# Kernel optimization log

Hardware: AMD Instinct MI355X
Metric: run time of the kernel (lower is better)

Reference implementation:

```python
import jax, jax.numpy as jnp
import numpy as np
from jax import lax

D_CONV = 4


def setup_inputs() -> dict:
    key = jax.random.key(0)
    ks = jax.random.split(key, 8)
    b, L, d_model = 2, 1024, 1024
    d_inner, d_state = 2048, 16
    s = 0.02  # weight scale
    return {
        "x": jax.random.normal(ks[0], (b, L, d_model), jnp.float32),
        "in_w": jax.random.normal(ks[1], (2 * d_inner, d_model), jnp.float32) * s,
        "in_b": jnp.zeros((2 * d_inner,), jnp.float32),
        "conv_w": jax.random.normal(ks[2], (d_inner, 1, D_CONV), jnp.float32) * s,
        "conv_b": jnp.zeros((d_inner,), jnp.float32),
        "xproj_w": jax.random.normal(ks[3], (2 * d_state + 1, d_inner), jnp.float32) * s,
        "dt_w": jax.random.normal(ks[4], (d_inner, 1), jnp.float32) * s,
        "dt_b": jnp.zeros((d_inner,), jnp.float32),
        "A_log": jax.random.normal(ks[5], (d_inner, d_state), jnp.float32),
        "D": jnp.ones((d_inner,), jnp.float32),
        "out_w": jax.random.normal(ks[6], (d_model, d_inner), jnp.float32) * s,
    }


def reference(x, in_w, in_b, conv_w, conv_b, xproj_w, dt_w, dt_b, A_log, D, out_w):
    b, L, _ = x.shape
    d_inner = conv_w.shape[0]
    d_state = A_log.shape[1]

    xz = x @ in_w.T + in_b                       # (b, L, 2*d_inner)
    xh, z = jnp.split(xz, 2, axis=-1)            # each (b, L, d_inner)

    # depthwise causal conv1d (torch pads d_conv-1 both sides then slices [:L])
    xc = jnp.transpose(xh, (0, 2, 1))            # (b, d_inner, L)
    xc = lax.conv_general_dilated(
        xc, conv_w, window_strides=(1,), padding=[(D_CONV - 1, 0)],
        feature_group_count=d_inner, dimension_numbers=("NCH", "OIH", "NCH"))
    xc = xc + conv_b[None, :, None]
    xh = jnp.transpose(xc, (0, 2, 1))            # (b, L, d_inner)

    xh = xh * jax.nn.silu(z)

    proj = xh @ xproj_w.T                        # (b, L, 2*d_state+1)
    dlt = proj[..., :1]                          # (b, L, 1)
    B = proj[..., 1:1 + d_state]                 # (b, L, d_state)
    C = proj[..., 1 + d_state:]                  # (b, L, d_state)

    # dt_proj: (b,L,1) -> (b,L,d_inner); source applies softplus then exp
    delta = jnp.exp(jax.nn.softplus(dlt @ dt_w.T + dt_b))  # (b, L, d_inner)

    A = -jnp.exp(A_log)                          # (d_inner, d_state)

    def step(h, inp):
        xt, dt, Bt, Ct = inp                     # (b,i), (b,i), (b,s), (b,s)
        A_bar = jnp.exp(A[None] * dt[..., None])          # (b, i, s)
        B_bar = dt[..., None] * Bt[:, None, :]            # (b, i, s)
        h = A_bar * h + B_bar * xt[..., None]             # (b, i, s)
        yt = jnp.einsum("bis,bs->bi", h, Ct)              # (b, i)
        return h, yt

    h0 = jnp.zeros((b, d_inner, d_state), x.dtype)
    xs = (jnp.moveaxis(xh, 1, 0), jnp.moveaxis(delta, 1, 0),
          jnp.moveaxis(B, 1, 0), jnp.moveaxis(C, 1, 0))
    _, ys = lax.scan(step, h0, xs)               # (L, b, d_inner)
    y = jnp.moveaxis(ys, 0, 1) + D * xh          # (b, L, d_inner)

    return y @ out_w.T                           # (b, L, d_model)
```

## Files before the change

kernel.cpp:

```cpp
#include <hip/hip_runtime.h>
#include <hip/hip_bf16.h>

#define NTOK   2048
#define DMODEL 1024
#define DINNER 2048
#define DSTATE 16
#define SEQLEN 1024
#define NPROJ  33
#define NPAD   48
#define KSPLIT 16
#define CCH    64
#define CT     16

typedef __attribute__((ext_vector_type(8))) short bf16x8;
typedef __attribute__((ext_vector_type(4))) float f32x4;
typedef __attribute__((ext_vector_type(8))) unsigned short us8;

__device__ __forceinline__ unsigned short f2bf(float f) {
  unsigned u = __float_as_uint(f);
  return (unsigned short)((u + 0x7FFFu + ((u >> 16) & 1u)) >> 16);
}

__device__ __forceinline__ void gload_lds16(const void* g, void* l) {
  __builtin_amdgcn_global_load_lds(
      (const __attribute__((address_space(1))) unsigned int*)g,
      (__attribute__((address_space(3))) unsigned int*)l, 16, 0, 0);
}

#define CAST_N0 (NTOK * DMODEL)
#define CAST_N1 (CAST_N0 + 2 * DINNER * DMODEL)
#define CAST_N2 (CAST_N1 + DMODEL * DINNER)
#define CAST_N3 (CAST_N2 + NPAD * DINNER)
__global__ __launch_bounds__(256) void cast4_bf16_kernel(
    const float* __restrict__ s0, const float* __restrict__ s1,
    const float* __restrict__ s2, const float* __restrict__ s3,
    unsigned short* __restrict__ dst) {
  const int idx = (blockIdx.x * 256 + threadIdx.x) * 8;
  const float* src;
  int off;
  if (idx < CAST_N0) { src = s0; off = idx; }
  else if (idx < CAST_N1) { src = s1; off = idx - CAST_N0; }
  else if (idx < CAST_N2) { src = s2; off = idx - CAST_N1; }
  else {
    off = idx - CAST_N2;
    if (off >= NPROJ * DINNER) {
      us8 z = {0, 0, 0, 0, 0, 0, 0, 0};
      *(us8*)(dst + idx) = z;
      return;
    }
    src = s3;
  }
  const float4 a = *(const float4*)(src + off);
  const float4 b = *(const float4*)(src + off + 4);
  us8 o;
  o[0] = f2bf(a.x); o[1] = f2bf(a.y); o[2] = f2bf(a.z); o[3] = f2bf(a.w);
  o[4] = f2bf(b.x); o[5] = f2bf(b.y); o[6] = f2bf(b.z); o[7] = f2bf(b.w);
  *(us8*)(dst + idx) = o;
}

template <int BN>
__global__ __launch_bounds__(256) void gemm_bt_mfma(
    const unsigned short* __restrict__ A, const unsigned short* __restrict__ B,
    const float* __restrict__ bias, float* __restrict__ C, int M, int K) {
  constexpr int TN = BN / 32;
  __shared__ unsigned short As[2][128 * 32];
  __shared__ unsigned short Bs[2][BN * 32];

  const int tid = threadIdx.x;
  const int wid = tid >> 6;
  const int lane = tid & 63;
  const int n0 = blockIdx.x * 128;
  const int m0 = blockIdx.y * BN;

  const int wave_m = wid & 1;
  const int wave_n = wid >> 1;
  const int lm = lane & 15;
  const int lq = lane >> 4;

  f32x4 acc[4][TN] = {};

  for (int k0 = 0; k0 < K; k0 += 64) {
    __syncthreads();
#pragma unroll
    for (int h = 0; h < 2; ++h) {
      const int kh = k0 + h * 32;
#pragma unroll
      for (int j = 0; j < 2; ++j) {
        const int cb = j * 256 + wid * 64;
        const int c = cb + lane;
        gload_lds16(A + (size_t)(n0 + (c >> 2)) * K + kh + (c & 3) * 8,
                    &As[h][cb * 8]);
      }
#pragma unroll
      for (int j = 0; j < BN / 64; ++j) {
        const int cb = j * 256 + wid * 64;
        const int c = cb + lane;
        gload_lds16(B + (size_t)(m0 + (c >> 2)) * K + kh + (c & 3) * 8,
                    &Bs[h][cb * 8]);
      }
    }
    __syncthreads();

#pragma unroll
    for (int h = 0; h < 2; ++h) {
      bf16x8 af[4], bfr[TN];
#pragma unroll
      for (int tm = 0; tm < 4; ++tm)
        af[tm] = *(const bf16x8*)
            &As[h][(wave_m * 64 + tm * 16 + lm) * 32 + lq * 8];
#pragma unroll
      for (int tn = 0; tn < TN; ++tn)
        bfr[tn] = *(const bf16x8*)
            &Bs[h][(wave_n * (BN / 2) + tn * 16 + lm) * 32 + lq * 8];
#pragma unroll
      for (int tm = 0; tm < 4; ++tm)
#pragma unroll
        for (int tn = 0; tn < TN; ++tn)
          acc[tm][tn] = __builtin_amdgcn_mfma_f32_16x16x32_bf16(
              af[tm], bfr[tn], acc[tm][tn], 0, 0, 0);
    }
  }

#pragma unroll
  for (int tm = 0; tm < 4; ++tm) {
    const int row = n0 + wave_m * 64 + tm * 16 + lq * 4;
#pragma unroll
    for (int tn = 0; tn < TN; ++tn) {
      const int col = m0 + wave_n * (BN / 2) + tn * 16 + lm;
      const float bv = bias ? bias[col] : 0.f;
#pragma unroll
      for (int r = 0; r < 4; ++r)
        C[(size_t)(row + r) * M + col] = acc[tm][tn][r] + bv;
    }
  }
}

__global__ __launch_bounds__(256) void conv_gate_kernel(
    const float* __restrict__ xz, const float* __restrict__ cw,
    const float* __restrict__ cb, float* __restrict__ xg,
    unsigned short* __restrict__ xgb) {
  const int i = blockIdx.y * 256 + threadIdx.x;
  const int n0 = blockIdx.x * 4;
  const int l0 = n0 & (SEQLEN - 1);

  const float4 w4 = ((const float4*)cw)[i];
  const float cbv = cb[i];
  float taps[7];
#pragma unroll
  for (int d = 0; d < 7; ++d) {
    const bool valid = (l0 != 0) || (d >= 3);
    taps[d] = valid ? xz[(size_t)(n0 - 3 + d) * (2 * DINNER) + i] : 0.f;
  }
#pragma unroll
  for (int tok = 0; tok < 4; ++tok) {
    float acc = cbv;
    acc = fmaf(w4.x, taps[tok + 0], acc);
    acc = fmaf(w4.y, taps[tok + 1], acc);
    acc = fmaf(w4.z, taps[tok + 2], acc);
    acc = fmaf(w4.w, taps[tok + 3], acc);
    const float z = xz[(size_t)(n0 + tok) * (2 * DINNER) + DINNER + i];
    const float sig = 1.f / (1.f + __expf(-z));
    const float v = acc * (z * sig);
    const size_t o = (size_t)(n0 + tok) * DINNER + i;
    xg[o] = v;
    xgb[o] = f2bf(v);
  }
}

__global__ __launch_bounds__(256) void xproj_mfma_kernel(
    const unsigned short* __restrict__ xgb, const unsigned short* __restrict__ wp,
    float* __restrict__ pp) {
  __shared__ unsigned short As[128 * 32];
  __shared__ unsigned short Bs[NPAD * 32];

  const int tid = threadIdx.x;
  const int wid = tid >> 6;
  const int lane = tid & 63;
  const int n0 = blockIdx.x * 128;
  const int kbase = blockIdx.y * (DINNER / KSPLIT);

  const int lm = lane & 15;
  const int lq = lane >> 4;

  f32x4 acc[2][3] = {};

  for (int it = 0; it < (DINNER / KSPLIT) / 32; ++it) {
    const int k0 = kbase + it * 32;
    __syncthreads();
#pragma unroll
    for (int j = 0; j < 2; ++j) {
      const int cb = j * 256 + wid * 64;
      const int c = cb + lane;
      gload_lds16(xgb + (size_t)(n0 + (c >> 2)) * DINNER + k0 + (c & 3) * 8,
                  &As[cb * 8]);
    }
    if (wid < 3) {
      const int cb = wid * 64;
      const int c = cb + lane;
      gload_lds16(wp + (size_t)(c >> 2) * DINNER + k0 + (c & 3) * 8,
                  &Bs[cb * 8]);
    }
    __syncthreads();

    bf16x8 af[2], bfr[3];
#pragma unroll
    for (int tm = 0; tm < 2; ++tm)
      af[tm] = *(const bf16x8*)&As[(wid * 32 + tm * 16 + lm) * 32 + lq * 8];
#pragma unroll
    for (int tn = 0; tn < 3; ++tn)
      bfr[tn] = *(const bf16x8*)&Bs[(tn * 16 + lm) * 32 + lq * 8];
#pragma unroll
    for (int tm = 0; tm < 2; ++tm)
#pragma unroll
      for (int tn = 0; tn < 3; ++tn)
        acc[tm][tn] = __builtin_amdgcn_mfma_f32_16x16x32_bf16(
            af[tm], bfr[tn], acc[tm][tn], 0, 0, 0);
  }

  float* base = pp + (size_t)blockIdx.y * NTOK * NPAD;
#pragma unroll
  for (int tm = 0; tm < 2; ++tm) {
    const int row = n0 + wid * 32 + tm * 16 + lq * 4;
#pragma unroll
    for (int tn = 0; tn < 3; ++tn) {
      const int col = tn * 16 + lm;
#pragma unroll
      for (int r = 0; r < 4; ++r)
        base[(size_t)(row + r) * NPAD + col] = acc[tm][tn][r];
    }
  }
}

__global__ __launch_bounds__(256) void proj_reduce_kernel(
    const float* __restrict__ pp, float* __restrict__ proj) {
  const int gid = blockIdx.x * 256 + threadIdx.x;
  if (gid >= NTOK * NPROJ) return;
  const int n = gid / NPROJ;
  const int r = gid - n * NPROJ;
  float s = 0.f;
#pragma unroll
  for (int q = 0; q < KSPLIT; ++q)
    s += pp[((size_t)q * NTOK + n) * NPAD + r];
  proj[gid] = s;
}

__global__ __launch_bounds__(256) void scan_phase1(
    const float* __restrict__ xg, const float* __restrict__ proj,
    const float* __restrict__ dt_w, const float* __restrict__ dt_b,
    const float* __restrict__ A_log,
    float* __restrict__ Sbuf, float* __restrict__ Hbuf) {
  __shared__ float pl[CT][36];
  const int tid = threadIdx.x;
  const int i = blockIdx.x * 256 + tid;
  const int k = blockIdx.y;
  const int b = blockIdx.z;
  const int n0 = b * SEQLEN + k * CT;

  for (int e = tid; e < CT * NPROJ; e += 256) {
    const int t = e / NPROJ;
    const int c = e - t * NPROJ;
    pl[t][c] = proj[(size_t)(n0 + t) * NPROJ + c];
  }
  __syncthreads();

  const float dtw = dt_w[i], dtb = dt_b[i];
  float Av[DSTATE];
#pragma unroll
  for (int s = 0; s < DSTATE; ++s) Av[s] = -__expf(A_log[i * DSTATE + s]);

  float h[DSTATE] = {};
  float Ssum = 0.f;

  for (int t = 0; t < CT; ++t) {
    float fr[20];
#pragma unroll
    for (int j = 0; j < 5; ++j) {
      const float4 v = *(const float4*)&pl[t][j * 4];
      fr[4 * j + 0] = v.x; fr[4 * j + 1] = v.y;
      fr[4 * j + 2] = v.z; fr[4 * j + 3] = v.w;
    }
    const float delta = 1.f + __expf(fmaf(fr[0], dtw, dtb));
    Ssum += delta;
    const float x = xg[(size_t)(n0 + t) * DINNER + i];
    const float dx = delta * x;
#pragma unroll
    for (int s = 0; s < DSTATE; ++s)
      h[s] = fmaf(__expf(Av[s] * delta), h[s], fr[1 + s] * dx);
  }

  const size_t ck = (size_t)(b * CCH + k) * DINNER + i;
  Sbuf[ck] = Ssum;
  float4* Hq = (float4*)(Hbuf + ck * DSTATE);
#pragma unroll
  for (int q = 0; q < 4; ++q)
    Hq[q] = make_float4(h[4 * q], h[4 * q + 1], h[4 * q + 2], h[4 * q + 3]);
}

__global__ __launch_bounds__(256) void scan_phase2(
    const float* __restrict__ A_log, const float* __restrict__ Sbuf,
    float* __restrict__ Hbuf) {
  const int gid = blockIdx.x * 256 + threadIdx.x;
  const int s = gid & (DSTATE - 1);
  const int i = (gid >> 4) & (DINNER - 1);
  const int b = gid >> 15;
  const float Av = -__expf(A_log[i * DSTATE + s]);
  float H = 0.f;
  for (int k = 0; k < CCH; ++k) {
    const size_t ck = (size_t)(b * CCH + k) * DINNER + i;
    const float hk = Hbuf[ck * DSTATE + s];
    const float a = __expf(Av * Sbuf[ck]);
    Hbuf[ck * DSTATE + s] = H;
    H = fmaf(a, H, hk);
  }
}

__global__ __launch_bounds__(256) void scan_phase3(
    const float* __restrict__ xg, const float* __restrict__ proj,
    const float* __restrict__ dt_w, const float* __restrict__ dt_b,
    const float* __restrict__ A_log, const float* __restrict__ Dp,
    const float* __restrict__ Hbuf, unsigned short* __restrict__ y) {
  __shared__ float pl[CT][36];
  const int tid = threadIdx.x;
  const int i = blockIdx.x * 256 + tid;
  const int k = blockIdx.y;
  const int b = blockIdx.z;
  const int n0 = b * SEQLEN + k * CT;

  for (int e = tid; e < CT * NPROJ; e += 256) {
    const int t = e / NPROJ;
    const int c = e - t * NPROJ;
    pl[t][c] = proj[(size_t)(n0 + t) * NPROJ + c];
  }
  __syncthreads();

  const float dtw = dt_w[i], dtb = dt_b[i];
  const float Dv = Dp[i];
  float Av[DSTATE];
#pragma unroll
  for (int s = 0; s < DSTATE; ++s) Av[s] = -__expf(A_log[i * DSTATE + s]);

  const size_t ck = (size_t)(b * CCH + k) * DINNER + i;
  float h[DSTATE];
  const float4* Hq = (const float4*)(Hbuf + ck * DSTATE);
#pragma unroll
  for (int q = 0; q < 4; ++q) {
    const float4 v = Hq[q];
    h[4 * q + 0] = v.x; h[4 * q + 1] = v.y;
    h[4 * q + 2] = v.z; h[4 * q + 3] = v.w;
  }

  for (int t = 0; t < CT; ++t) {
    float fr[33];
#pragma unroll
    for (int j = 0; j < 8; ++j) {
      const float4 v = *(const float4*)&pl[t][j * 4];
      fr[4 * j + 0] = v.x; fr[4 * j + 1] = v.y;
      fr[4 * j + 2] = v.z; fr[4 * j + 3] = v.w;
    }
    fr[32] = pl[t][32];
    const float delta = 1.f + __expf(fmaf(fr[0], dtw, dtb));
    const float x = xg[(size_t)(n0 + t) * DINNER + i];
    const float dx = delta * x;
    float yt = 0.f;
#pragma unroll
    for (int s = 0; s < DSTATE; ++s) {
      h[s] = fmaf(__expf(Av[s] * delta), h[s], fr[1 + s] * dx);
      yt = fmaf(h[s], fr[17 + s], yt);
    }
    y[(size_t)(n0 + t) * DINNER + i] = f2bf(fmaf(Dv, x, yt));
  }
}

extern "C" void kernel_launch(void* const* d_in, const int* in_sizes, int n_in,
                              void* d_out, int out_size, void* d_ws, size_t ws_size,
                              hipStream_t stream) {
  const float* x       = (const float*)d_in[0];
  const float* in_w    = (const float*)d_in[1];
  const float* in_b    = (const float*)d_in[2];
  const float* conv_w  = (const float*)d_in[3];
  const float* conv_b  = (const float*)d_in[4];
  const float* xproj_w = (const float*)d_in[5];
  const float* dt_w    = (const float*)d_in[6];
  const float* dt_b    = (const float*)d_in[7];
  const float* A_log   = (const float*)d_in[8];
  const float* Dp      = (const float*)d_in[9];
  const float* out_w   = (const float*)d_in[10];
  float* out = (float*)d_out;

  float* ws = (float*)d_ws;
  float* xz = ws;
  float* xg = ws + 8388608;
  unsigned short* xgb = (unsigned short*)(ws + 12582912);
  unsigned short* bf_base = (unsigned short*)(ws + 14680064);
  unsigned short* x_bf    = bf_base;
  unsigned short* inw_bf  = bf_base + CAST_N0;
  unsigned short* outw_bf = bf_base + CAST_N1;
  unsigned short* wpad_bf = bf_base + CAST_N2;
  unsigned short* yb_bf = (unsigned short*)(ws + 19398656);
  float* pp   = ws + 20971520;
  float* proj = ws + 22544384;
  float* Sbuf = ws + 23068672;
  float* Hbuf = ws + 23592960;

  cast4_bf16_kernel<<<CAST_N3 / (256 * 8), 256, 0, stream>>>(
      x, in_w, out_w, xproj_w, bf_base);

  gemm_bt_mfma<128><<<dim3(NTOK / 128, (2 * DINNER) / 128), 256, 0, stream>>>(
      x_bf, inw_bf, in_b, xz, 2 * DINNER, DMODEL);

  conv_gate_kernel<<<dim3(NTOK / 4, DINNER / 256), 256, 0, stream>>>(
      xz, conv_w, conv_b, xg, xgb);

  xproj_mfma_kernel<<<dim3(NTOK / 128, KSPLIT), 256, 0, stream>>>(
      xgb, wpad_bf, pp);
  proj_reduce_kernel<<<(NTOK * NPROJ + 255) / 256, 256, 0, stream>>>(pp, proj);

  scan_phase1<<<dim3(DINNER / 256, CCH, 2), 256, 0, stream>>>(
      xg, proj, dt_w, dt_b, A_log, Sbuf, Hbuf);
  scan_phase2<<<(2 * DINNER * DSTATE) / 256, 256, 0, stream>>>(
      A_log, Sbuf, Hbuf);
  scan_phase3<<<dim3(DINNER / 256, CCH, 2), 256, 0, stream>>>(
      xg, proj, dt_w, dt_b, A_log, Dp, Hbuf, yb_bf);

  gemm_bt_mfma<64><<<dim3(NTOK / 128, DMODEL / 64), 256, 0, stream>>>(
      yb_bf, outw_bf, nullptr, out, DMODEL, DINNER);
}
```

Baseline: 222.7 us.

## Fuse conv-gate into x-projection GEMM and split-K the output projection with atomics

The depthwise conv plus SiLU gate now runs inside the x-projection kernel. It writes the bf16 gated activations straight into shared memory as the MFMA A tile, which removes the separate conv kernel, the xgb global buffer, the split-K partial buffer and the reduction kernel. Partial projections are accumulated into proj with atomicAdd after a memset. The output GEMM uses a 2-way split-K with atomicAdd into a zeroed output to double the block count. The cost is two memsets, atomic traffic, and a conv loop that walks 64 tokens per thread sequentially, with less parallelism than the old conv kernel.

```diff
diff --git a/kernel.cpp b/kernel.cpp
--- a/kernel.cpp
+++ b/kernel.cpp
@@ -8,7 +8,6 @@
 #define SEQLEN 1024
 #define NPROJ  33
 #define NPAD   48
-#define KSPLIT 16
 #define CCH    64
 #define CT     16
 
@@ -58,11 +57,10 @@
   *(us8*)(dst + idx) = o;
 }
 
-template <int BN>
 __global__ __launch_bounds__(256) void gemm_bt_mfma(
     const unsigned short* __restrict__ A, const unsigned short* __restrict__ B,
     const float* __restrict__ bias, float* __restrict__ C, int M, int K) {
-  constexpr int TN = BN / 32;
+  constexpr int BN = 128, TN = 4;
   __shared__ unsigned short As[2][128 * 32];
   __shared__ unsigned short Bs[2][BN * 32];
 
@@ -127,7 +125,7 @@
 #pragma unroll
     for (int tn = 0; tn < TN; ++tn) {
       const int col = m0 + wave_n * (BN / 2) + tn * 16 + lm;
-      const float bv = bias ? bias[col] : 0.f;
+      const float bv = bias[col];
 #pragma unroll
       for (int r = 0; r < 4; ++r)
         C[(size_t)(row + r) * M + col] = acc[tm][tn][r] + bv;
@@ -135,80 +133,147 @@
   }
 }
 
-__global__ __launch_bounds__(256) void conv_gate_kernel(
-    const float* __restrict__ xz, const float* __restrict__ cw,
-    const float* __restrict__ cb, float* __restrict__ xg,
-    unsigned short* __restrict__ xgb) {
-  const int i = blockIdx.y * 256 + threadIdx.x;
-  const int n0 = blockIdx.x * 4;
-  const int l0 = n0 & (SEQLEN - 1);
-
-  const float4 w4 = ((const float4*)cw)[i];
-  const float cbv = cb[i];
-  float taps[7];
-#pragma unroll
-  for (int d = 0; d < 7; ++d) {
-    const bool valid = (l0 != 0) || (d >= 3);
-    taps[d] = valid ? xz[(size_t)(n0 - 3 + d) * (2 * DINNER) + i] : 0.f;
-  }
-#pragma unroll
-  for (int tok = 0; tok < 4; ++tok) {
-    float acc = cbv;
-    acc = fmaf(w4.x, taps[tok + 0], acc);
-    acc = fmaf(w4.y, taps[tok + 1], acc);
-    acc = fmaf(w4.z, taps[tok + 2], acc);
-    acc = fmaf(w4.w, taps[tok + 3], acc);
-    const float z = xz[(size_t)(n0 + tok) * (2 * DINNER) + DINNER + i];
-    const float sig = 1.f / (1.f + __expf(-z));
-    const float v = acc * (z * sig);
-    const size_t o = (size_t)(n0 + tok) * DINNER + i;
-    xg[o] = v;
-    xgb[o] = f2bf(v);
-  }
-}
-
-__global__ __launch_bounds__(256) void xproj_mfma_kernel(
-    const unsigned short* __restrict__ xgb, const unsigned short* __restrict__ wp,
-    float* __restrict__ pp) {
-  __shared__ unsigned short As[128 * 32];
-  __shared__ unsigned short Bs[NPAD * 32];
+__global__ __launch_bounds__(256) void gemm_bt_mfma_sk(
+    const unsigned short* __restrict__ A, const unsigned short* __restrict__ B,
+    float* __restrict__ C, int M, int K) {
+  constexpr int BN = 64, TN = 2;
+  __shared__ unsigned short As[2][128 * 32];
+  __shared__ unsigned short Bs[2][BN * 32];
 
   const int tid = threadIdx.x;
   const int wid = tid >> 6;
   const int lane = tid & 63;
   const int n0 = blockIdx.x * 128;
-  const int kbase = blockIdx.y * (DINNER / KSPLIT);
-
+  const int m0 = blockIdx.y * BN;
+  const int kstart = blockIdx.z * (K >> 1);
+
+  const int wave_m = wid & 1;
+  const int wave_n = wid >> 1;
   const int lm = lane & 15;
   const int lq = lane >> 4;
 
+  f32x4 acc[4][TN] = {};
+
+  for (int k0 = kstart; k0 < kstart + (K >> 1); k0 += 64) {
+    __syncthreads();
+#pragma unroll
+    for (int h = 0; h < 2; ++h) {
+      const int kh = k0 + h * 32;
+#pragma unroll
+      for (int j = 0; j < 2; ++j) {
+        const int cb = j * 256 + wid * 64;
+        const int c = cb + lane;
+        gload_lds16(A + (size_t)(n0 + (c >> 2)) * K + kh + (c & 3) * 8,
+                    &As[h][cb * 8]);
+      }
+      {
+        const int cb = wid * 64;
+        const int c = cb + lane;
+        gload_lds16(B + (size_t)(m0 + (c >> 2)) * K + kh + (c & 3) * 8,
+                    &Bs[h][cb * 8]);
+      }
+    }
+    __syncthreads();
+
+#pragma unroll
+    for (int h = 0; h < 2; ++h) {
+      bf16x8 af[4], bfr[TN];
+#pragma unroll
+      for (int tm = 0; tm < 4; ++tm)
+        af[tm] = *(const bf16x8*)
+            &As[h][(wave_m * 64 + tm * 16 + lm) * 32 + lq * 8];
+#pragma unroll
+      for (int tn = 0; tn < TN; ++tn)
+        bfr[tn] = *(const bf16x8*)
+            &Bs[h][(wave_n * (BN / 2) + tn * 16 + lm) * 32 + lq * 8];
+#pragma unroll
+      for (int tm = 0; tm < 4; ++tm)
+#pragma unroll
+        for (int tn = 0; tn < TN; ++tn)
+          acc[tm][tn] = __builtin_amdgcn_mfma_f32_16x16x32_bf16(
+              af[tm], bfr[tn], acc[tm][tn], 0, 0, 0);
+    }
+  }
+
+#pragma unroll
+  for (int tm = 0; tm < 4; ++tm) {
+    const int row = n0 + wave_m * 64 + tm * 16 + lq * 4;
+#pragma unroll
+    for (int tn = 0; tn < TN; ++tn) {
+      const int col = m0 + wave_n * (BN / 2) + tn * 16 + lm;
+#pragma unroll
+      for (int r = 0; r < 4; ++r)
+        atomicAdd(&C[(size_t)(row + r) * M + col], acc[tm][tn][r]);
+    }
+  }
+}
+
+__global__ __launch_bounds__(256) void conv_xproj_mfma(
+    const float* __restrict__ xz, const float* __restrict__ cw,
+    const float* __restrict__ cb, const unsigned short* __restrict__ wp,
+    float* __restrict__ xg, float* __restrict__ proj) {
+  __shared__ unsigned short As[4][128 * 32];
+  __shared__ unsigned short Bs[4][NPAD * 32];
+
+  const int tid = threadIdx.x;
+  const int wid = tid >> 6;
+  const int lane = tid & 63;
+  const int n0 = blockIdx.x * 128;
+  const int kb = blockIdx.y * 128;
+
+#pragma unroll
+  for (int j = 0; j < 3; ++j) {
+    const int cbase = j * 256 + wid * 64;
+    const int c = cbase + lane;
+    const int stage = c / 192;
+    const int rem = c - stage * 192;
+    gload_lds16(wp + (size_t)(rem >> 2) * DINNER + kb + stage * 32 + (rem & 3) * 8,
+                &Bs[0][0] + cbase * 8);
+  }
+
+  const int c128 = tid & 127;
+  const int half = tid >> 7;
+  const int i = kb + c128;
+  const int gt0 = n0 + half * 64;
+  const float4 w4 = ((const float4*)cw)[i];
+  const float cbv = cb[i];
+
+  const bool seq_start = ((gt0 & (SEQLEN - 1)) == 0);
+  float tm3 = seq_start ? 0.f : xz[(size_t)(gt0 - 3) * (2 * DINNER) + i];
+  float tm2 = seq_start ? 0.f : xz[(size_t)(gt0 - 2) * (2 * DINNER) + i];
+  float tm1 = seq_start ? 0.f : xz[(size_t)(gt0 - 1) * (2 * DINNER) + i];
+
+  unsigned short* Arow = &As[c128 >> 5][c128 & 31];
+#pragma unroll 4
+  for (int t = 0; t < 64; ++t) {
+    const int n = gt0 + t;
+    const float x0 = xz[(size_t)n * (2 * DINNER) + i];
+    float acc = cbv;
+    acc = fmaf(w4.x, tm3, acc);
+    acc = fmaf(w4.y, tm2, acc);
+    acc = fmaf(w4.z, tm1, acc);
+    acc = fmaf(w4.w, x0, acc);
+    const float z = xz[(size_t)n * (2 * DINNER) + DINNER + i];
+    const float sig = 1.f / (1.f + __expf(-z));
+    const float v = acc * (z * sig);
+    xg[(size_t)n * DINNER + i] = v;
+    Arow[(half * 64 + t) * 32] = f2bf(v);
+    tm3 = tm2; tm2 = tm1; tm1 = x0;
+  }
+  __syncthreads();
+
+  const int lm = lane & 15;
+  const int lq = lane >> 4;
   f32x4 acc[2][3] = {};
-
-  for (int it = 0; it < (DINNER / KSPLIT) / 32; ++it) {
-    const int k0 = kbase + it * 32;
-    __syncthreads();
-#pragma unroll
-    for (int j = 0; j < 2; ++j) {
-      const int cb = j * 256 + wid * 64;
-      const int c = cb + lane;
-      gload_lds16(xgb + (size_t)(n0 + (c >> 2)) * DINNER + k0 + (c & 3) * 8,
-                  &As[cb * 8]);
-    }
-    if (wid < 3) {
-      const int cb = wid * 64;
-      const int c = cb + lane;
-      gload_lds16(wp + (size_t)(c >> 2) * DINNER + k0 + (c & 3) * 8,
-                  &Bs[cb * 8]);
-    }
-    __syncthreads();
-
+#pragma unroll
+  for (int stage = 0; stage < 4; ++stage) {
     bf16x8 af[2], bfr[3];
 #pragma unroll
     for (int tm = 0; tm < 2; ++tm)
-      af[tm] = *(const bf16x8*)&As[(wid * 32 + tm * 16 + lm) * 32 + lq * 8];
+      af[tm] = *(const bf16x8*)&As[stage][(wid * 32 + tm * 16 + lm) * 32 + lq * 8];
 #pragma unroll
     for (int tn = 0; tn < 3; ++tn)
-      bfr[tn] = *(const bf16x8*)&Bs[(tn * 16 + lm) * 32 + lq * 8];
+      bfr[tn] = *(const bf16x8*)&Bs[stage][(tn * 16 + lm) * 32 + lq * 8];
 #pragma unroll
     for (int tm = 0; tm < 2; ++tm)
 #pragma unroll
@@ -217,31 +282,19 @@
             af[tm], bfr[tn], acc[tm][tn], 0, 0, 0);
   }
 
-  float* base = pp + (size_t)blockIdx.y * NTOK * NPAD;
 #pragma unroll
   for (int tm = 0; tm < 2; ++tm) {
     const int row = n0 + wid * 32 + tm * 16 + lq * 4;
 #pragma unroll
     for (int tn = 0; tn < 3; ++tn) {
       const int col = tn * 16 + lm;
-#pragma unroll
-      for (int r = 0; r < 4; ++r)
-        base[(size_t)(row + r) * NPAD + col] = acc[tm][tn][r];
-    }
-  }
-}
-
-__global__ __launch_bounds__(256) void proj_reduce_kernel(
-    const float* __restrict__ pp, float* __restrict__ proj) {
-  const int gid = blockIdx.x * 256 + threadIdx.x;
-  if (gid >= NTOK * NPROJ) return;
-  const int n = gid / NPROJ;
-  const int r = gid - n * NPROJ;
-  float s = 0.f;
-#pragma unroll
-  for (int q = 0; q < KSPLIT; ++q)
-    s += pp[((size_t)q * NTOK + n) * NPAD + r];
-  proj[gid] = s;
+      if (col < NPROJ) {
+#pragma unroll
+        for (int r = 0; r < 4; ++r)
+          atomicAdd(&proj[(size_t)(row + r) * NPROJ + col], acc[tm][tn][r]);
+      }
+    }
+  }
 }
 
 __global__ __launch_bounds__(256) void scan_phase1(
@@ -390,30 +443,26 @@
   float* ws = (float*)d_ws;
   float* xz = ws;
   float* xg = ws + 8388608;
-  unsigned short* xgb = (unsigned short*)(ws + 12582912);
-  unsigned short* bf_base = (unsigned short*)(ws + 14680064);
+  unsigned short* bf_base = (unsigned short*)(ws + 12582912);
   unsigned short* x_bf    = bf_base;
   unsigned short* inw_bf  = bf_base + CAST_N0;
   unsigned short* outw_bf = bf_base + CAST_N1;
   unsigned short* wpad_bf = bf_base + CAST_N2;
-  unsigned short* yb_bf = (unsigned short*)(ws + 19398656);
-  float* pp   = ws + 20971520;
-  float* proj = ws + 22544384;
-  float* Sbuf = ws + 23068672;
-  float* Hbuf = ws + 23592960;
-
+  unsigned short* yb_bf = (unsigned short*)(ws + 16826368);
+  float* proj = ws + 18923520;
+  float* Sbuf = ws + 19005440;
+  float* Hbuf = ws + 19267584;
+
+  hipMemsetAsync(proj, 0, (size_t)NTOK * NPROJ * 4, stream);
+  hipMemsetAsync(out, 0, (size_t)NTOK * DMODEL * 4, stream);
   cast4_bf16_kernel<<<CAST_N3 / (256 * 8), 256, 0, stream>>>(
       x, in_w, out_w, xproj_w, bf_base);
 
-  gemm_bt_mfma<128><<<dim3(NTOK / 128, (2 * DINNER) / 128), 256, 0, stream>>>(
+  gemm_bt_mfma<<<dim3(NTOK / 128, (2 * DINNER) / 128), 256, 0, stream>>>(
       x_bf, inw_bf, in_b, xz, 2 * DINNER, DMODEL);
 
-  conv_gate_kernel<<<dim3(NTOK / 4, DINNER / 256), 256, 0, stream>>>(
-      xz, conv_w, conv_b, xg, xgb);
-
-  xproj_mfma_kernel<<<dim3(NTOK / 128, KSPLIT), 256, 0, stream>>>(
-      xgb, wpad_bf, pp);
-  proj_reduce_kernel<<<(NTOK * NPROJ + 255) / 256, 256, 0, stream>>>(pp, proj);
+  conv_xproj_mfma<<<dim3(NTOK / 128, DINNER / 128), 256, 0, stream>>>(
+      xz, conv_w, conv_b, wpad_bf, xg, proj);
 
   scan_phase1<<<dim3(DINNER / 256, CCH, 2), 256, 0, stream>>>(
       xg, proj, dt_w, dt_b, A_log, Sbuf, Hbuf);
@@ -422,6 +471,6 @@
   scan_phase3<<<dim3(DINNER / 256, CCH, 2), 256, 0, stream>>>(
       xg, proj, dt_w, dt_b, A_log, Dp, Hbuf, yb_bf);
 
-  gemm_bt_mfma<64><<<dim3(NTOK / 128, DMODEL / 64), 256, 0, stream>>>(
-      yb_bf, outw_bf, nullptr, out, DMODEL, DINNER);
-}
+  gemm_bt_mfma_sk<<<dim3(NTOK / 128, DMODEL / 64, 2), 256, 0, stream>>>(
+      yb_bf, outw_bf, out, DMODEL, DINNER);
+}
```

After: 224.7 us. No clear change (+0.9%).
